# Kernel tuning notes

Hardware: AMD Instinct MI355X
Metric: run time of the kernel (lower is better)

Reference implementation:

```python
import jax, jax.numpy as jnp
import numpy as np

FACTOR = 1.0
KERNEL = 3
PAD = 1
STRIDE = 1


def setup_inputs() -> dict:
    key = jax.random.key(0)
    ks = jax.random.split(key, 7)
    B_, Cin, Cout, L, CODE = 32, 128, 128, 4096, 2
    return {
        "input": jax.random.normal(ks[0], (B_, Cin, L), dtype=jnp.float32),
        "codes": jax.random.normal(ks[1], (B_, CODE, CODE), dtype=jnp.float32),
        "weight": jax.random.normal(ks[2], (Cout, Cin, KERNEL), dtype=jnp.float32) * 0.05,
        "A": jax.random.normal(ks[3], (Cin, CODE, KERNEL), dtype=jnp.float32) * 0.05,
        "B": jax.random.normal(ks[4], (Cout, CODE, KERNEL), dtype=jnp.float32) * 0.05,
        "bias": jax.random.normal(ks[5], (Cout,), dtype=jnp.float32) * 0.05,
        "bias_context": jax.random.normal(ks[6], (CODE, Cout), dtype=jnp.float32) * 0.05,
    }


def reference(input, codes, weight, A, B, bias, bias_context):
    # Hypernetwork-generated per-sample conv weights (low-rank via codes)
    w = jnp.einsum('ick,bcr->birk', A, codes)            # (b, in, code, k)
    context_w = jnp.einsum('birk,ork->boik', w, B)       # (b, out, in, k)
    combined_weight = weight + FACTOR * context_w        # (b, out, in, k)

    diag = jnp.diagonal(codes, axis1=-2, axis2=-1)       # (b, code)
    context_bias = diag @ bias_context                   # (b, out)
    combined_bias = bias + FACTOR * context_bias         # (b, out)

    # circular padding along spatial axis
    padded = jnp.pad(input, ((0, 0), (0, 0), (PAD, PAD)), mode='wrap')
    L_out = (input.shape[-1] + 2 * PAD - KERNEL) // STRIDE + 1
    # windowed view: (b, in, L_out, k) via k shifted slices (k is tiny, loop ok)
    windows = jnp.stack([padded[:, :, j:j + L_out * STRIDE:STRIDE] for j in range(KERNEL)], axis=-1)
    out = jnp.einsum('bihw,boiw->boh', windows, combined_weight)
    return out + combined_bias[..., None]
```

## Files before the change

### kernel.cpp

```cpp
#include <hip/hip_runtime.h>
#include <hip/hip_bf16.h>
#include <stdint.h>
#include <stddef.h>

#define L_LEN 4096
#define CIN   128
#define COUT  128
#define NB    32
#define KTOT  384
#define TN    64
#define TPB   4
#define ROWS  (TN + 2)

typedef __bf16 bf16x8 __attribute__((ext_vector_type(8)));
typedef float  f32x4  __attribute__((ext_vector_type(4)));

__device__ __forceinline__ uint16_t f2bf(float f) {
    union { float f; uint32_t u; } v; v.f = f;
    return (uint16_t)((v.u + 0x7fffu + ((v.u >> 16) & 1u)) >> 16);
}
__device__ __forceinline__ uint32_t pack2(float lo, float hi) {
    return (uint32_t)f2bf(lo) | ((uint32_t)f2bf(hi) << 16);
}

__global__ __launch_bounds__(256) void geps_combine(
    const float* __restrict__ codes, const float* __restrict__ weight,
    const float* __restrict__ Amat,  const float* __restrict__ Bmat,
    const float* __restrict__ bias,  const float* __restrict__ bias_ctx,
    uint16_t* __restrict__ Wc, float* __restrict__ cbias)
{
    int tid = blockIdx.x * 256 + threadIdx.x;
    if (tid < NB * COUT * KTOT) {
        int j    = tid & 7;
        int lane = (tid >> 3) & 63;
        int mt   = (tid >> 9) & 1;
        int tmp  = tid >> 10;
        int t    = tmp % 12;
        int bo   = tmp / 12;
        int og   = bo & 3;
        int b    = bo >> 2;
        int col  = t * 32 + (lane >> 4) * 8 + j;
        int k    = col >> 7;
        int i    = col & 127;
        int o    = og * 32 + mt * 16 + (lane & 15);
        float cw = 0.f;
        #pragma unroll
        for (int c = 0; c < 2; ++c) {
            float a = Amat[i * 6 + c * 3 + k];
            #pragma unroll
            for (int r = 0; r < 2; ++r)
                cw += a * codes[b * 4 + c * 2 + r] * Bmat[o * 6 + r * 3 + k];
        }
        float val = weight[o * 384 + i * 3 + k] + cw;
        Wc[tid] = f2bf(val);
    }
    if (tid < NB * COUT) {
        int b = tid >> 7, o = tid & 127;
        float cb = bias[o];
        #pragma unroll
        for (int c = 0; c < 2; ++c)
            cb += codes[b * 4 + c * 2 + c] * bias_ctx[c * 128 + o];
        cbias[tid] = cb;
    }
}

#define LOAD_TILE(H0)                                                        \
    {                                                                        \
        const float* tb = inb + (H0);                                        \
        _Pragma("unroll")                                                    \
        for (int it = 0; it < 2; ++it) {                                     \
            int task = it * 256 + tid;                                       \
            int p4   = task >> 4;                                            \
            int qd   = task & 15;                                            \
            const float* r0 = tb + (size_t)(4 * p4) * L_LEN + 4 * qd;        \
            st[it][0] = *(const float4*)(r0);                                \
            st[it][1] = *(const float4*)(r0 + L_LEN);                        \
            st[it][2] = *(const float4*)(r0 + 2 * L_LEN);                    \
            st[it][3] = *(const float4*)(r0 + 3 * L_LEN);                    \
        }                                                                    \
        if (tid < 128) {                                                     \
            int p    = tid & 63;                                             \
            int side = tid >> 6;                                             \
            int r    = side ? (ROWS - 1) : 0;                                \
            int gh   = ((H0) - 1 + r) & (L_LEN - 1);                         \
            hx0 = inb[(size_t)(2 * p) * L_LEN + gh];                         \
            hx1 = inb[(size_t)(2 * p + 1) * L_LEN + gh];                     \
        }                                                                    \
    }

#define PACK_TILE(XP)                                                        \
    {                                                                        \
        uint16_t* Xw = (XP);                                                 \
        _Pragma("unroll")                                                    \
        for (int it = 0; it < 2; ++it) {                                     \
            int task = it * 256 + tid;                                       \
            int p4   = task >> 4;                                            \
            int qd   = task & 15;                                            \
            const int off = (4 * p4) & 7;                                    \
            const int pc  = p4 >> 1;                                         \
            _Pragma("unroll")                                                \
            for (int j4 = 0; j4 < 4; ++j4) {                                 \
                int r  = 1 + 4 * qd + j4;                                    \
                int ch = pc ^ (r & 15);                                      \
                uint2 w;                                                     \
                w.x = pack2(((const float*)&st[it][0])[j4],                  \
                            ((const float*)&st[it][1])[j4]);                 \
                w.y = pack2(((const float*)&st[it][2])[j4],                  \
                            ((const float*)&st[it][3])[j4]);                 \
                *(uint2*)&Xw[r * 128 + (ch << 3) + off] = w;                 \
            }                                                                \
        }                                                                    \
        if (tid < 128) {                                                     \
            int p     = tid & 63;                                            \
            int side  = tid >> 6;                                            \
            int r     = side ? (ROWS - 1) : 0;                               \
            int chunk = (p >> 2) ^ (r & 15);                                 \
            *(uint32_t*)&Xw[r * 128 + (chunk << 3) + ((2 * p) & 7)] =        \
                pack2(hx0, hx1);                                             \
        }                                                                    \
    }

__global__ __launch_bounds__(256, 2) void geps_conv(
    const float* __restrict__ in, const uint16_t* __restrict__ Wc,
    const float* __restrict__ cbias, float* __restrict__ out)
{
    __shared__ uint16_t __attribute__((aligned(16))) Xt[2][ROWS * 128];
    __shared__ float cb[COUT];

    const int tid  = threadIdx.x;
    const int b    = blockIdx.y;
    const int hb   = blockIdx.x * (TN * TPB);
    const int lane = tid & 63;
    const int wid  = tid >> 6;
    const int m16  = lane & 15;
    const int q    = lane >> 4;
    const int mq   = wid * 32;

    if (tid < COUT) cb[tid] = cbias[b * COUT + tid];

    const float* inb = in + (size_t)b * CIN * L_LEN;

    const uint16_t* WcW = Wc + (size_t)(b * 4 + wid) * 12288 + lane * 8;
    bf16x8 af[12][2];
    #pragma unroll
    for (int t = 0; t < 12; ++t) {
        af[t][0] = *(const bf16x8*)(WcW + t * 1024);
        af[t][1] = *(const bf16x8*)(WcW + t * 1024 + 512);
    }

    float4 st[2][4];
    float  hx0 = 0.f, hx1 = 0.f;

    LOAD_TILE(hb)
    PACK_TILE(&Xt[0][0])
    __syncthreads();

    f32x4 acc[2][4];

    #pragma unroll 1
    for (int j = 0; j < TPB; ++j) {
        const int h0 = hb + j * TN;
        const uint16_t* X = &Xt[j & 1][0];

        if (j + 1 < TPB) LOAD_TILE(h0 + TN)
        asm volatile("" ::: "memory");

        #pragma unroll
        for (int a = 0; a < 2; ++a)
            #pragma unroll
            for (int c = 0; c < 4; ++c) acc[a][c] = 0.0f;

        #pragma unroll
        for (int t = 0; t < 12; ++t) {
            const int k   = t >> 2;
            const int i0c = (t & 3) << 2;
            bf16x8 bfv[4];
            #pragma unroll
            for (int nt = 0; nt < 4; ++nt) {
                int r  = nt * 16 + m16 + k;
                int ch = (i0c + q) ^ (r & 15);
                bfv[nt] = *(const bf16x8*)&X[r * 128 + (ch << 3)];
            }
            #pragma unroll
            for (int nt = 0; nt < 4; ++nt) {
                acc[0][nt] = __builtin_amdgcn_mfma_f32_16x16x32_bf16(
                    af[t][0], bfv[nt], acc[0][nt], 0, 0, 0);
                acc[1][nt] = __builtin_amdgcn_mfma_f32_16x16x32_bf16(
                    af[t][1], bfv[nt], acc[1][nt], 0, 0, 0);
            }
        }

        float* outb = out + (size_t)b * COUT * L_LEN + h0;
        #pragma unroll
        for (int mt = 0; mt < 2; ++mt) {
            #pragma unroll
            for (int reg = 0; reg < 4; ++reg) {
                int o = mq + mt * 16 + q * 4 + reg;
                float bv = cb[o];
                float* orow = outb + (size_t)o * L_LEN;
                #pragma unroll
                for (int nt = 0; nt < 4; ++nt)
                    __builtin_nontemporal_store(acc[mt][nt][reg] + bv,
                                                &orow[nt * 16 + m16]);
            }
        }

        if (j + 1 < TPB) {
            PACK_TILE(&Xt[(j + 1) & 1][0])
            __syncthreads();
        }
    }
}

extern "C" void kernel_launch(void* const* d_in, const int* in_sizes, int n_in,
                              void* d_out, int out_size, void* d_ws, size_t ws_size,
                              hipStream_t stream) {
    const float* input    = (const float*)d_in[0];
    const float* codes    = (const float*)d_in[1];
    const float* weight   = (const float*)d_in[2];
    const float* Amat     = (const float*)d_in[3];
    const float* Bmat     = (const float*)d_in[4];
    const float* bias     = (const float*)d_in[5];
    const float* bias_ctx = (const float*)d_in[6];
    float* out = (float*)d_out;

    uint16_t* Wc    = (uint16_t*)d_ws;
    float*    cbias = (float*)((char*)d_ws + (size_t)NB * COUT * KTOT * 2);

    geps_combine<<<dim3((NB * COUT * KTOT) / 256), 256, 0, stream>>>(
        codes, weight, Amat, Bmat, bias, bias_ctx, Wc, cbias);
    geps_conv<<<dim3(L_LEN / (TN * TPB), NB), 256, 0, stream>>>(
        input, Wc, cbias, out);
}
```

Baseline: 140.9 us.

## Stream weight fragments from global and split tile prefetch into halves

The kernel no longer keeps all 24 bf16x8 weight fragments in registers for its whole life. It reloads them from global/L2 one step ahead inside the MFMA loop. The next-tile prefetch is split into two halves, with load and pack interleaved between the two halves of the MFMA work, which halves the float4 staging registers. The aim is to cut VGPR pressure, possibly raising occupancy or avoiding spills, at the cost of re-reading weights on every tile and adding global loads to the compute loop.

```diff
diff --git a/kernel.cpp b/kernel.cpp
--- a/kernel.cpp
+++ b/kernel.cpp
@@ -64,59 +64,82 @@
     }
 }
 
-#define LOAD_TILE(H0)                                                        \
+
+#define LOAD_HALF(IT, H0)                                                    \
     {                                                                        \
-        const float* tb = inb + (H0);                                        \
+        int L_p4 = ((IT) << 4) + (tid >> 4);                                 \
+        int L_qd = tid & 15;                                                 \
+        const float* L_r0 = inb + (size_t)(4 * L_p4) * L_LEN + (H0) + 4 * L_qd; \
+        st[0] = *(const float4*)(L_r0);                                      \
+        st[1] = *(const float4*)(L_r0 + L_LEN);                              \
+        st[2] = *(const float4*)(L_r0 + 2 * L_LEN);                          \
+        st[3] = *(const float4*)(L_r0 + 3 * L_LEN);                          \
+        if ((IT) && tid < 128) {                                             \
+            int L_p    = tid & 63;                                           \
+            int L_side = tid >> 6;                                           \
+            int L_r    = L_side ? (ROWS - 1) : 0;                            \
+            int L_gh   = ((H0) - 1 + L_r) & (L_LEN - 1);                     \
+            hx0 = inb[(size_t)(2 * L_p) * L_LEN + L_gh];                     \
+            hx1 = inb[(size_t)(2 * L_p + 1) * L_LEN + L_gh];                 \
+        }                                                                    \
+    }
+
+#define PACK_HALF(IT, XP)                                                    \
+    {                                                                        \
+        uint16_t* P_Xw = (XP);                                               \
+        int P_p4 = ((IT) << 4) + (tid >> 4);                                 \
+        int P_qd = tid & 15;                                                 \
+        const int P_off = (4 * P_p4) & 7;                                    \
+        const int P_pc  = P_p4 >> 1;                                         \
         _Pragma("unroll")                                                    \
-        for (int it = 0; it < 2; ++it) {                                     \
-            int task = it * 256 + tid;                                       \
-            int p4   = task >> 4;                                            \
-            int qd   = task & 15;                                            \
-            const float* r0 = tb + (size_t)(4 * p4) * L_LEN + 4 * qd;        \
-            st[it][0] = *(const float4*)(r0);                                \
-            st[it][1] = *(const float4*)(r0 + L_LEN);                        \
-            st[it][2] = *(const float4*)(r0 + 2 * L_LEN);                    \
-            st[it][3] = *(const float4*)(r0 + 3 * L_LEN);                    \
-        }                                                                    \
-        if (tid < 128) {                                                     \
-            int p    = tid & 63;                                             \
-            int side = tid >> 6;                                             \
-            int r    = side ? (ROWS - 1) : 0;                                \
-            int gh   = ((H0) - 1 + r) & (L_LEN - 1);                         \
-            hx0 = inb[(size_t)(2 * p) * L_LEN + gh];                         \
-            hx1 = inb[(size_t)(2 * p + 1) * L_LEN + gh];                     \
-        }                                                                    \
-    }
-
-#define PACK_TILE(XP)                                                        \
+        for (int P_j4 = 0; P_j4 < 4; ++P_j4) {                               \
+            int P_r  = 1 + 4 * P_qd + P_j4;                                  \
+            int P_ch = P_pc ^ (P_r & 15);                                    \
+            uint2 P_w;                                                       \
+            P_w.x = pack2(((const float*)&st[0])[P_j4],                      \
+                          ((const float*)&st[1])[P_j4]);                     \
+            P_w.y = pack2(((const float*)&st[2])[P_j4],                      \
+                          ((const float*)&st[3])[P_j4]);                     \
+            *(uint2*)&P_Xw[P_r * 128 + (P_ch << 3) + P_off] = P_w;           \
+        }                                                                    \
+        if ((IT) && tid < 128) {                                             \
+            int P_p     = tid & 63;                                          \
+            int P_side  = tid >> 6;                                          \
+            int P_hr    = P_side ? (ROWS - 1) : 0;                           \
+            int P_chunk = (P_p >> 2) ^ (P_hr & 15);                          \
+            *(uint32_t*)&P_Xw[P_hr * 128 + (P_chunk << 3) + ((2 * P_p) & 7)] = \
+                pack2(hx0, hx1);                                             \
+        }                                                                    \
+    }
+
+#define KHALF(T0, XR)                                                        \
     {                                                                        \
-        uint16_t* Xw = (XP);                                                 \
+        const uint16_t* K_X = (XR);                                          \
+        bf16x8 K_a0 = *(const bf16x8*)(WcW + (T0) * 1024);                   \
+        bf16x8 K_a1 = *(const bf16x8*)(WcW + (T0) * 1024 + 512);             \
         _Pragma("unroll")                                                    \
-        for (int it = 0; it < 2; ++it) {                                     \
-            int task = it * 256 + tid;                                       \
-            int p4   = task >> 4;                                            \
-            int qd   = task & 15;                                            \
-            const int off = (4 * p4) & 7;                                    \
-            const int pc  = p4 >> 1;                                         \
+        for (int K_tt = 0; K_tt < 6; ++K_tt) {                               \
+            const int K_t  = (T0) + K_tt;                                    \
+            const int K_tn = (K_t + 1 < 12) ? (K_t + 1) : 11;                \
+            bf16x8 K_n0 = *(const bf16x8*)(WcW + K_tn * 1024);               \
+            bf16x8 K_n1 = *(const bf16x8*)(WcW + K_tn * 1024 + 512);         \
+            const int K_k   = K_t >> 2;                                      \
+            const int K_i0c = (K_t & 3) << 2;                                \
+            bf16x8 K_bfv[4];                                                 \
             _Pragma("unroll")                                                \
-            for (int j4 = 0; j4 < 4; ++j4) {                                 \
-                int r  = 1 + 4 * qd + j4;                                    \
-                int ch = pc ^ (r & 15);                                      \
-                uint2 w;                                                     \
-                w.x = pack2(((const float*)&st[it][0])[j4],                  \
-                            ((const float*)&st[it][1])[j4]);                 \
-                w.y = pack2(((const float*)&st[it][2])[j4],                  \
-                            ((const float*)&st[it][3])[j4]);                 \
-                *(uint2*)&Xw[r * 128 + (ch << 3) + off] = w;                 \
+            for (int K_nt = 0; K_nt < 4; ++K_nt) {                           \
+                int K_r  = K_nt * 16 + m16 + K_k;                            \
+                int K_ch = (K_i0c + q) ^ (K_r & 15);                         \
+                K_bfv[K_nt] = *(const bf16x8*)&K_X[K_r * 128 + (K_ch << 3)]; \
             }                                                                \
-        }                                                                    \
-        if (tid < 128) {                                                     \
-            int p     = tid & 63;                                            \
-            int side  = tid >> 6;                                            \
-            int r     = side ? (ROWS - 1) : 0;                               \
-            int chunk = (p >> 2) ^ (r & 15);                                 \
-            *(uint32_t*)&Xw[r * 128 + (chunk << 3) + ((2 * p) & 7)] =        \
-                pack2(hx0, hx1);                                             \
+            _Pragma("unroll")                                                \
+            for (int K_nt = 0; K_nt < 4; ++K_nt) {                           \
+                acc[0][K_nt] = __builtin_amdgcn_mfma_f32_16x16x32_bf16(      \
+                    K_a0, K_bfv[K_nt], acc[0][K_nt], 0, 0, 0);               \
+                acc[1][K_nt] = __builtin_amdgcn_mfma_f32_16x16x32_bf16(      \
+                    K_a1, K_bfv[K_nt], acc[1][K_nt], 0, 0, 0);               \
+            }                                                                \
+            K_a0 = K_n0; K_a1 = K_n1;                                        \
         }                                                                    \
     }
 
@@ -139,30 +162,26 @@
     if (tid < COUT) cb[tid] = cbias[b * COUT + tid];
 
     const float* inb = in + (size_t)b * CIN * L_LEN;
-
     const uint16_t* WcW = Wc + (size_t)(b * 4 + wid) * 12288 + lane * 8;
-    bf16x8 af[12][2];
-    #pragma unroll
-    for (int t = 0; t < 12; ++t) {
-        af[t][0] = *(const bf16x8*)(WcW + t * 1024);
-        af[t][1] = *(const bf16x8*)(WcW + t * 1024 + 512);
-    }
-
-    float4 st[2][4];
+
+    float4 st[4];
     float  hx0 = 0.f, hx1 = 0.f;
-
-    LOAD_TILE(hb)
-    PACK_TILE(&Xt[0][0])
+    f32x4  acc[2][4];
+
+    LOAD_HALF(0, hb)
+    PACK_HALF(0, &Xt[0][0])
+    LOAD_HALF(1, hb)
+    PACK_HALF(1, &Xt[0][0])
     __syncthreads();
-
-    f32x4 acc[2][4];
 
     #pragma unroll 1
     for (int j = 0; j < TPB; ++j) {
         const int h0 = hb + j * TN;
-        const uint16_t* X = &Xt[j & 1][0];
-
-        if (j + 1 < TPB) LOAD_TILE(h0 + TN)
+        uint16_t* Xcur = &Xt[j & 1][0];
+        uint16_t* Xnxt = &Xt[(j + 1) & 1][0];
+        const bool pre = (j + 1 < TPB);
+
+        if (pre) LOAD_HALF(0, h0 + TN)
         asm volatile("" ::: "memory");
 
         #pragma unroll
@@ -170,25 +189,15 @@
             #pragma unroll
             for (int c = 0; c < 4; ++c) acc[a][c] = 0.0f;
 
-        #pragma unroll
-        for (int t = 0; t < 12; ++t) {
-            const int k   = t >> 2;
-            const int i0c = (t & 3) << 2;
-            bf16x8 bfv[4];
-            #pragma unroll
-            for (int nt = 0; nt < 4; ++nt) {
-                int r  = nt * 16 + m16 + k;
-                int ch = (i0c + q) ^ (r & 15);
-                bfv[nt] = *(const bf16x8*)&X[r * 128 + (ch << 3)];
-            }
-            #pragma unroll
-            for (int nt = 0; nt < 4; ++nt) {
-                acc[0][nt] = __builtin_amdgcn_mfma_f32_16x16x32_bf16(
-                    af[t][0], bfv[nt], acc[0][nt], 0, 0, 0);
-                acc[1][nt] = __builtin_amdgcn_mfma_f32_16x16x32_bf16(
-                    af[t][1], bfv[nt], acc[1][nt], 0, 0, 0);
-            }
+        KHALF(0, Xcur)
+
+        if (pre) {
+            PACK_HALF(0, Xnxt)
+            LOAD_HALF(1, h0 + TN)
+            asm volatile("" ::: "memory");
         }
+
+        KHALF(6, Xcur)
 
         float* outb = out + (size_t)b * COUT * L_LEN + h0;
         #pragma unroll
@@ -205,10 +214,8 @@
             }
         }
 
-        if (j + 1 < TPB) {
-            PACK_TILE(&Xt[(j + 1) & 1][0])
-            __syncthreads();
-        }
+        if (pre) PACK_HALF(1, Xnxt)
+        __syncthreads();
     }
 }
 
```

Result: slower. 147.9 us (+5.0%).
